# Kernel tuning notes

Hardware: AMD Instinct MI355X
Metric: run time of the kernel (lower is better)

Reference implementation:

```python
import jax, jax.numpy as jnp
import numpy as np

NUM_NODES = 100000
IN_DIM = 64
OUT_DIM = 64
NUM_EDGES = 1250000


def setup_inputs() -> dict:
    key = jax.random.key(0)
    k1, k2, k3, k4, k5 = jax.random.split(key, 5)
    x = jax.random.normal(k1, (NUM_NODES, IN_DIM), dtype=jnp.float32)
    edge_index = jax.random.randint(k2, (2, NUM_EDGES), 0, NUM_NODES, dtype=jnp.int32)
    # Linear params (PyTorch default init: uniform(-1/sqrt(in), 1/sqrt(in)))
    bound = 1.0 / np.sqrt(IN_DIM)
    W_self = jax.random.uniform(k3, (OUT_DIM, IN_DIM), minval=-bound, maxval=bound, dtype=jnp.float32)
    b_self = jax.random.uniform(k4, (OUT_DIM,), minval=-bound, maxval=bound, dtype=jnp.float32)
    W_neigh = jax.random.uniform(k5, (OUT_DIM, IN_DIM), minval=-bound, maxval=bound, dtype=jnp.float32)
    return {"x": x, "edge_index": edge_index, "W_self": W_self, "b_self": b_self, "W_neigh": W_neigh}


def reference(x, edge_index, W_self, b_self, W_neigh):
    # x: [N, D_in], edge_index: [2, E]
    src, dst = edge_index[0], edge_index[1]
    num_nodes = x.shape[0]
    x_src = x[src]  # [E, D_in] gather
    neigh_agg = jax.ops.segment_sum(x_src, dst, num_segments=num_nodes)  # [N, D_in]
    deg = jax.ops.segment_sum(jnp.ones_like(dst, dtype=x.dtype), dst, num_segments=num_nodes)
    deg = jnp.clip(deg, 1.0, None)[:, None]
    neigh_mean = neigh_agg / deg
    out = x @ W_self.T + b_self + neigh_mean @ W_neigh.T
    return jax.nn.relu(out)
```

## Files before the change

kernel.cpp:

```cpp
#include <hip/hip_runtime.h>


#define BKSH 9
#define BKN 512
#define NBMAX 256
#define CAPE 7168
#define WPT (CAPE / BKN)
#define CHUNK 4096
#define EPT (CHUNK / 256)

typedef __attribute__((ext_vector_type(8))) short short8;
typedef __attribute__((ext_vector_type(4))) float floatx4;

static __device__ inline unsigned short f2bf(float f) {
  union { float f; unsigned int u; } v;
  v.f = f;
  unsigned int r = v.u + 0x7FFFu + ((v.u >> 16) & 1u);
  return (unsigned short)(r >> 16);
}

static __device__ inline short8 pack8(float4 a, float4 b) {
  short8 s;
  s[0] = (short)f2bf(a.x); s[1] = (short)f2bf(a.y);
  s[2] = (short)f2bf(a.z); s[3] = (short)f2bf(a.w);
  s[4] = (short)f2bf(b.x); s[5] = (short)f2bf(b.y);
  s[6] = (short)f2bf(b.z); s[7] = (short)f2bf(b.w);
  return s;
}

static __device__ inline void add8(float* a, short8 sv) {
  union { short8 s; unsigned int u[4]; } c; c.s = sv;
#pragma unroll
  for (int i = 0; i < 4; ++i) {
    a[2 * i]     += __uint_as_float(c.u[i] << 16);
    a[2 * i + 1] += __uint_as_float(c.u[i] & 0xFFFF0000u);
  }
}

static __device__ inline void cvt8(float* a, short8 sv) {
  union { short8 s; unsigned int u[4]; } c; c.s = sv;
#pragma unroll
  for (int i = 0; i < 4; ++i) {
    a[2 * i]     = __uint_as_float(c.u[i] << 16);
    a[2 * i + 1] = __uint_as_float(c.u[i] & 0xFFFF0000u);
  }
}

__global__ __launch_bounds__(256) void k1_main(
    const float* __restrict__ x,
    const float* __restrict__ Wself, const float* __restrict__ bself,
    const float* __restrict__ Wneigh,
    unsigned short* __restrict__ yb, unsigned short* __restrict__ zb,
    const int* __restrict__ src, const int* __restrict__ dst,
    int* __restrict__ cursor, int* __restrict__ ebuf,
    int E, int N, int NB, int SCB) {
  __shared__ int h[NBMAX], loff[NBMAX], gbase[NBMAX];
  __shared__ int sbuf[CHUNK];
  int t = threadIdx.x;
  int bid = blockIdx.x;

  if (bid >= SCB) {
    int lane = t & 63;
    int w = t >> 6;
    int tb = (bid - SCB) * 64 + w * 16;
    int m = lane & 15, q = lane >> 4;
    unsigned short* lds  = (unsigned short*)sbuf;
    unsigned short* ylds = lds + w * 2048;
    unsigned short* zlds = ylds + 1024;

    long long rowA = (long long)min(tb + m, N - 1) * 64;
    short8 ax[2];
#pragma unroll
    for (int ks = 0; ks < 2; ++ks) {
      const float* xr = &x[rowA + ks * 32 + q * 8];
      ax[ks] = pack8(*(const float4*)xr, *(const float4*)(xr + 4));
    }

#pragma unroll
    for (int nt = 0; nt < 4; ++nt) {
      int ob = nt * 16;
      long long rowB = (long long)(ob + m) * 64;
      floatx4 accs = {0.f, 0.f, 0.f, 0.f};
      floatx4 accn = {0.f, 0.f, 0.f, 0.f};
#pragma unroll
      for (int ks = 0; ks < 2; ++ks) {
        const float* pw = &Wself[rowB + ks * 32 + q * 8];
        short8 bs = pack8(*(const float4*)pw, *(const float4*)(pw + 4));
        accs = __builtin_amdgcn_mfma_f32_16x16x32_bf16(ax[ks], bs, accs, 0, 0, 0);
        const float* pn = &Wneigh[rowB + ks * 32 + q * 8];
        short8 bn = pack8(*(const float4*)pn, *(const float4*)(pn + 4));
        accn = __builtin_amdgcn_mfma_f32_16x16x32_bf16(ax[ks], bn, accn, 0, 0, 0);
      }
      float bias = bself[ob + m];
#pragma unroll
      for (int r = 0; r < 4; ++r) {
        int nl = q * 4 + r;
        ylds[nl * 64 + ob + m] = f2bf(accs[r] + bias);
        zlds[nl * 64 + ob + m] = f2bf(accn[r]);
      }
    }
    if (tb + (lane >> 2) < N) {
      long long go = (long long)tb * 64 + lane * 16;
      *(short8*)&yb[go]     = *(short8*)&ylds[lane * 16];
      *(short8*)&yb[go + 8] = *(short8*)&ylds[lane * 16 + 8];
      *(short8*)&zb[go]     = *(short8*)&zlds[lane * 16];
      *(short8*)&zb[go + 8] = *(short8*)&zlds[lane * 16 + 8];
    }
    return;
  }

  int w = t >> 6, lane = t & 63;
  if (t < NBMAX) h[t] = 0;
  __syncthreads();

  int base = bid * CHUNK;
  int myd[EPT], mys[EPT];
#pragma unroll
  for (int i = 0; i < EPT; ++i) {
    int e = base + t + 256 * i;
    if (e < E) {
      myd[i] = dst[e];
      mys[i] = src[e];
      atomicAdd(&h[myd[i] >> BKSH], 1);
    } else myd[i] = -1;
  }
  __syncthreads();

  if (t < 64) {
    int i0 = 4 * t;
    int v0 = h[i0], v1 = h[i0 + 1], v2 = h[i0 + 2], v3 = h[i0 + 3];
    int s4 = v0 + v1 + v2 + v3, inc = s4;
#pragma unroll
    for (int off = 1; off < 64; off <<= 1) {
      int u = __shfl_up(inc, off, 64);
      if (t >= off) inc += u;
    }
    int ex = inc - s4;
    loff[i0] = ex; loff[i0 + 1] = ex + v0;
    loff[i0 + 2] = ex + v0 + v1; loff[i0 + 3] = ex + v0 + v1 + v2;
  }
  __syncthreads();

  if (t < NB) {
    if (h[t] > 0) gbase[t] = t * CAPE + atomicAdd(&cursor[t], h[t]);
  }
  __syncthreads();
  if (t < NBMAX) h[t] = 0;
  __syncthreads();

#pragma unroll
  for (int i = 0; i < EPT; ++i) {
    if (myd[i] >= 0) {
      int b = myd[i] >> BKSH;
      int p = atomicAdd(&h[b], 1);
      sbuf[loff[b] + p] = mys[i] | ((myd[i] & (BKN - 1)) << 17);
    }
  }
  __syncthreads();

  for (int b = w; b < NB; b += 4) {
    int c = h[b], lo = loff[b], go = gbase[b];
    for (int j = lane; j < c; j += 64)
      ebuf[go + j] = sbuf[lo + j];
  }
}

__global__ __launch_bounds__(512) void sb_csr(const int* __restrict__ cursor,
                                              const int* __restrict__ ebuf,
                                              int* __restrict__ col,
                                              int2* __restrict__ rowse, int N) {
  __shared__ int sbuf[CAPE];
  __shared__ int cnt[BKN];
  __shared__ int wsum[8];
  int b = blockIdx.x, t = threadIdx.x;
  int s = b * CAPE;
  int n = cursor[b];
  int e = s + n;

  int my[WPT];
#pragma unroll
  for (int i = 0; i < WPT; ++i) {
    int j = s + t + i * BKN;
    my[i] = (j < e) ? ebuf[j] : -1;
  }

  cnt[t] = 0;
  __syncthreads();
#pragma unroll
  for (int i = 0; i < WPT; ++i)
    if (my[i] >= 0) atomicAdd(&cnt[(my[i] >> 17) & (BKN - 1)], 1);
  __syncthreads();

  int v = cnt[t];
  int lane = t & 63, w = t >> 6;
  int inc = v;
#pragma unroll
  for (int o = 1; o < 64; o <<= 1) {
    int u = __shfl_up(inc, o, 64);
    if (lane >= o) inc += u;
  }
  if (lane == 63) wsum[w] = inc;
  __syncthreads();
  if (t < 8) {
    int s0 = wsum[t], incw = s0;
#pragma unroll
    for (int o = 1; o < 8; o <<= 1) {
      int u = __shfl_up(incw, o, 64);
      if (t >= o) incw += u;
    }
    wsum[t] = incw - s0;
  }
  __syncthreads();
  int ex = wsum[w] + inc - v;
  int node = (b << BKSH) + t;
  if (node < N) rowse[node] = make_int2(s + ex, v);
  __syncthreads();
  cnt[t] = ex;
  __syncthreads();

#pragma unroll
  for (int i = 0; i < WPT; ++i) {
    if (my[i] >= 0) {
      int nl = (my[i] >> 17) & (BKN - 1);
      int p = atomicAdd(&cnt[nl], 1);
      sbuf[p] = my[i] & 0x1FFFF;
    }
  }
  __syncthreads();

  for (int j = t; j < n; j += BKN) col[s + j] = sbuf[j];
}

__global__ __launch_bounds__(256) void gather_oct(
    const unsigned short* __restrict__ zb,
    const int2* __restrict__ rowse,
    const int* __restrict__ col,
    const unsigned short* __restrict__ yb,
    float* __restrict__ out, int N) {
  int t = threadIdx.x;
  int lane = t & 63, w = t >> 6;
  int o = lane >> 3, d = lane & 7;
  int node = blockIdx.x * 32 + w * 8 + o;

  int2 se = rowse[min(node, N - 1)];
  int s0 = se.x;
  int c = (node < N) ? se.y : 0;
  int cm1 = max(c - 1, 0);

  int cmax = c;
#pragma unroll
  for (int m = 8; m <= 32; m <<= 1) cmax = max(cmax, __shfl_xor(cmax, m, 64));

  long long ro = (long long)node * 64 + d * 8;
  long long ros = (long long)min(node, N - 1) * 64 + d * 8;
  short8 yv8 = *(const short8*)&yb[ros];

  float a[8] = {0.f, 0.f, 0.f, 0.f, 0.f, 0.f, 0.f, 0.f};
  float b2[8] = {0.f, 0.f, 0.f, 0.f, 0.f, 0.f, 0.f, 0.f};
  int colv = col[s0 + min(d, cm1)];
  for (int kb = 0; kb < cmax; kb += 8) {
    int colv_nx = 0;
    if (kb + 8 < cmax) colv_nx = col[s0 + min(kb + 8 + d, cm1)];
#pragma unroll
    for (int j = 0; j < 8; ++j) {
      bool p = (kb + j) < c;
      int cs = __shfl(colv, (lane & 56) | j, 64);
      cs = p ? cs : 0;
      short8 v = *(const short8*)&zb[(long long)cs * 64 + d * 8];
      if (p) add8((j & 1) ? b2 : a, v);
    }
    colv = colv_nx;
  }
#pragma unroll
  for (int k = 0; k < 8; ++k) a[k] += b2[k];

  if (node < N) {
    float inv = 1.0f / fmaxf((float)c, 1.0f);
    float yv[8];
    cvt8(yv, yv8);
    float4 r0, r1;
    r0.x = fmaxf(yv[0] + a[0] * inv, 0.f);
    r0.y = fmaxf(yv[1] + a[1] * inv, 0.f);
    r0.z = fmaxf(yv[2] + a[2] * inv, 0.f);
    r0.w = fmaxf(yv[3] + a[3] * inv, 0.f);
    r1.x = fmaxf(yv[4] + a[4] * inv, 0.f);
    r1.y = fmaxf(yv[5] + a[5] * inv, 0.f);
    r1.z = fmaxf(yv[6] + a[6] * inv, 0.f);
    r1.w = fmaxf(yv[7] + a[7] * inv, 0.f);
    *(float4*)&out[ro] = r0;
    *(float4*)&out[ro + 4] = r1;
  }
}

extern "C" void kernel_launch(void* const* d_in, const int* in_sizes, int n_in,
                              void* d_out, int out_size, void* d_ws, size_t ws_size,
                              hipStream_t stream) {
  const float* x      = (const float*)d_in[0];
  const int*   eidx   = (const int*)d_in[1];
  const float* Wself  = (const float*)d_in[2];
  const float* bself  = (const float*)d_in[3];
  const float* Wneigh = (const float*)d_in[4];
  float* out = (float*)d_out;

  const int N = in_sizes[0] / 64;
  const int E = in_sizes[1] / 2;
  const int* src = eidx;
  const int* dst = eidx + E;
  const int NB = (N + BKN - 1) / BKN;
  const int SCB = (E + CHUNK - 1) / CHUNK;

  unsigned short* yb = (unsigned short*)d_ws;
  unsigned short* zb = yb + (size_t)N * 64;
  int* cursor = (int*)(zb + (size_t)N * 64);
  int2* rowse = (int2*)(cursor + NBMAX);
  int* ebuf   = (int*)(rowse + N);
  int* col    = ebuf + (size_t)NB * CAPE;

  hipMemsetAsync(cursor, 0, NBMAX * sizeof(int), stream);

  const int GB = (N + 63) / 64;
  k1_main<<<SCB + GB, 256, 0, stream>>>(x, Wself, bself, Wneigh, yb, zb,
                                        src, dst, cursor, ebuf, E, N, NB, SCB);
  sb_csr<<<NB, BKN, 0, stream>>>(cursor, ebuf, col, rowse, N);
  gather_oct<<<(N + 31) / 32, 256, 0, stream>>>(zb, rowse, col, yb, out, N);
}
```

Measured before the change: 156.5 us.

## Co-schedule dense GEMM with per-bucket CSR build instead of edge scatter

Moves the dense x·W projection blocks out of the edge-scatter kernel and into the bucket CSR-building kernel, which now runs at 512 threads with 128 rows per GEMM block. The scatter kernel runs alone, and the GEMM work overlaps the CSR sort instead. The aim is better load balance, since the CSR stage launched only a few hundred blocks and left the GPU underused. The cost is a larger shared-memory footprint per block and a change in which kernel carries the GEMM latency.

```diff
diff --git a/kernel.cpp b/kernel.cpp
--- a/kernel.cpp
+++ b/kernel.cpp
@@ -46,25 +46,88 @@
   }
 }
 
-__global__ __launch_bounds__(256) void k1_main(
+__global__ __launch_bounds__(256) void k_scatter(
+    const int* __restrict__ src, const int* __restrict__ dst,
+    int* __restrict__ cursor, int* __restrict__ ebuf,
+    int E, int NB) {
+  __shared__ int h[NBMAX], loff[NBMAX], gbase[NBMAX];
+  __shared__ int sbuf[CHUNK];
+  int t = threadIdx.x;
+  int bid = blockIdx.x;
+  int w = t >> 6, lane = t & 63;
+
+  if (t < NBMAX) h[t] = 0;
+  __syncthreads();
+
+  int base = bid * CHUNK;
+  int myd[EPT], mys[EPT];
+#pragma unroll
+  for (int i = 0; i < EPT; ++i) {
+    int e = base + t + 256 * i;
+    if (e < E) {
+      myd[i] = dst[e];
+      mys[i] = src[e];
+      atomicAdd(&h[myd[i] >> BKSH], 1);
+    } else myd[i] = -1;
+  }
+  __syncthreads();
+
+  if (t < 64) {
+    int i0 = 4 * t;
+    int v0 = h[i0], v1 = h[i0 + 1], v2 = h[i0 + 2], v3 = h[i0 + 3];
+    int s4 = v0 + v1 + v2 + v3, inc = s4;
+#pragma unroll
+    for (int off = 1; off < 64; off <<= 1) {
+      int u = __shfl_up(inc, off, 64);
+      if (t >= off) inc += u;
+    }
+    int ex = inc - s4;
+    loff[i0] = ex; loff[i0 + 1] = ex + v0;
+    loff[i0 + 2] = ex + v0 + v1; loff[i0 + 3] = ex + v0 + v1 + v2;
+  }
+  __syncthreads();
+
+  if (t < NB) {
+    if (h[t] > 0) gbase[t] = t * CAPE + atomicAdd(&cursor[t], h[t]);
+  }
+  __syncthreads();
+  if (t < NBMAX) h[t] = 0;
+  __syncthreads();
+
+#pragma unroll
+  for (int i = 0; i < EPT; ++i) {
+    if (myd[i] >= 0) {
+      int b = myd[i] >> BKSH;
+      int p = atomicAdd(&h[b], 1);
+      sbuf[loff[b] + p] = mys[i] | ((myd[i] & (BKN - 1)) << 17);
+    }
+  }
+  __syncthreads();
+
+  for (int b = w; b < NB; b += 4) {
+    int c = h[b], lo = loff[b], go = gbase[b];
+    for (int j = lane; j < c; j += 64)
+      ebuf[go + j] = sbuf[lo + j];
+  }
+}
+
+__global__ __launch_bounds__(512) void k_gemm_csr(
     const float* __restrict__ x,
     const float* __restrict__ Wself, const float* __restrict__ bself,
     const float* __restrict__ Wneigh,
     unsigned short* __restrict__ yb, unsigned short* __restrict__ zb,
-    const int* __restrict__ src, const int* __restrict__ dst,
-    int* __restrict__ cursor, int* __restrict__ ebuf,
-    int E, int N, int NB, int SCB) {
-  __shared__ int h[NBMAX], loff[NBMAX], gbase[NBMAX];
-  __shared__ int sbuf[CHUNK];
+    const int* __restrict__ cursor, const int* __restrict__ ebuf,
+    int* __restrict__ col, int2* __restrict__ rowse,
+    int N, int NB) {
+  __shared__ int shm[8192];
   int t = threadIdx.x;
   int bid = blockIdx.x;
-
-  if (bid >= SCB) {
-    int lane = t & 63;
-    int w = t >> 6;
-    int tb = (bid - SCB) * 64 + w * 16;
+  int lane = t & 63, w = t >> 6;
+
+  if (bid >= NB) {
+    int tb = (bid - NB) * 128 + w * 16;
     int m = lane & 15, q = lane >> 4;
-    unsigned short* lds  = (unsigned short*)sbuf;
+    unsigned short* lds  = (unsigned short*)shm;
     unsigned short* ylds = lds + w * 2048;
     unsigned short* zlds = ylds + 1024;
 
@@ -109,70 +172,10 @@
     return;
   }
 
-  int w = t >> 6, lane = t & 63;
-  if (t < NBMAX) h[t] = 0;
-  __syncthreads();
-
-  int base = bid * CHUNK;
-  int myd[EPT], mys[EPT];
-#pragma unroll
-  for (int i = 0; i < EPT; ++i) {
-    int e = base + t + 256 * i;
-    if (e < E) {
-      myd[i] = dst[e];
-      mys[i] = src[e];
-      atomicAdd(&h[myd[i] >> BKSH], 1);
-    } else myd[i] = -1;
-  }
-  __syncthreads();
-
-  if (t < 64) {
-    int i0 = 4 * t;
-    int v0 = h[i0], v1 = h[i0 + 1], v2 = h[i0 + 2], v3 = h[i0 + 3];
-    int s4 = v0 + v1 + v2 + v3, inc = s4;
-#pragma unroll
-    for (int off = 1; off < 64; off <<= 1) {
-      int u = __shfl_up(inc, off, 64);
-      if (t >= off) inc += u;
-    }
-    int ex = inc - s4;
-    loff[i0] = ex; loff[i0 + 1] = ex + v0;
-    loff[i0 + 2] = ex + v0 + v1; loff[i0 + 3] = ex + v0 + v1 + v2;
-  }
-  __syncthreads();
-
-  if (t < NB) {
-    if (h[t] > 0) gbase[t] = t * CAPE + atomicAdd(&cursor[t], h[t]);
-  }
-  __syncthreads();
-  if (t < NBMAX) h[t] = 0;
-  __syncthreads();
-
-#pragma unroll
-  for (int i = 0; i < EPT; ++i) {
-    if (myd[i] >= 0) {
-      int b = myd[i] >> BKSH;
-      int p = atomicAdd(&h[b], 1);
-      sbuf[loff[b] + p] = mys[i] | ((myd[i] & (BKN - 1)) << 17);
-    }
-  }
-  __syncthreads();
-
-  for (int b = w; b < NB; b += 4) {
-    int c = h[b], lo = loff[b], go = gbase[b];
-    for (int j = lane; j < c; j += 64)
-      ebuf[go + j] = sbuf[lo + j];
-  }
-}
-
-__global__ __launch_bounds__(512) void sb_csr(const int* __restrict__ cursor,
-                                              const int* __restrict__ ebuf,
-                                              int* __restrict__ col,
-                                              int2* __restrict__ rowse, int N) {
-  __shared__ int sbuf[CAPE];
-  __shared__ int cnt[BKN];
-  __shared__ int wsum[8];
-  int b = blockIdx.x, t = threadIdx.x;
+  int* sbuf = shm;
+  int* cnt  = shm + CAPE;
+  int* wsum = shm + CAPE + BKN;
+  int b = bid;
   int s = b * CAPE;
   int n = cursor[b];
   int e = s + n;
@@ -192,7 +195,6 @@
   __syncthreads();
 
   int v = cnt[t];
-  int lane = t & 63, w = t >> 6;
   int inc = v;
 #pragma unroll
   for (int o = 1; o < 64; o <<= 1) {
@@ -318,9 +320,9 @@
 
   hipMemsetAsync(cursor, 0, NBMAX * sizeof(int), stream);
 
-  const int GB = (N + 63) / 64;
-  k1_main<<<SCB + GB, 256, 0, stream>>>(x, Wself, bself, Wneigh, yb, zb,
-                                        src, dst, cursor, ebuf, E, N, NB, SCB);
-  sb_csr<<<NB, BKN, 0, stream>>>(cursor, ebuf, col, rowse, N);
+  const int GB = (N + 127) / 128;
+  k_scatter<<<SCB, 256, 0, stream>>>(src, dst, cursor, ebuf, E, NB);
+  k_gemm_csr<<<NB + GB, 512, 0, stream>>>(x, Wself, bself, Wneigh, yb, zb,
+                                          cursor, ebuf, col, rowse, N, NB);
   gather_oct<<<(N + 31) / 32, 256, 0, stream>>>(zb, rowse, col, yb, out, N);
 }
```

Result: slower. 170.5 us (+9.0%).
